# Optimization experiments

Measured on AMD Instinct MI355X. Metric: run time of the kernel, lower is better.

The kernel has to match this reference:

```python
import jax, jax.numpy as jnp
import numpy as np
from jax import lax


def conv2d(x, w, b=None, stride=1, pad=0):
    y = lax.conv_general_dilated(x, w, (stride, stride), [(pad, pad), (pad, pad)],
                                 dimension_numbers=('NCHW', 'OIHW', 'NCHW'))
    if b is not None:
        y = y + b[None, :, None, None]
    return y


def bilinear_resize_ac(S, Ho, Wo):
    # F.interpolate(..., mode='bilinear', align_corners=True)
    B, C, H, W = S.shape
    ys = jnp.linspace(0.0, H - 1.0, Ho)
    xs = jnp.linspace(0.0, W - 1.0, Wo)
    y0 = jnp.floor(ys).astype(jnp.int32); y1 = jnp.minimum(y0 + 1, H - 1); wy = ys - y0
    x0 = jnp.floor(xs).astype(jnp.int32); x1 = jnp.minimum(x0 + 1, W - 1); wx = xs - x0
    Sy = S[:, :, y0, :] * (1 - wy)[None, None, :, None] + S[:, :, y1, :] * wy[None, None, :, None]
    return Sy[:, :, :, x0] * (1 - wx)[None, None, None, :] + Sy[:, :, :, x1] * wx[None, None, None, :]


def deform_conv(x, offset, weight, bias=None, mask=None, stride=1, pad=1, dil=1):
    # (Modulated) deformable conv, deformable_groups=1; DCNv2 semantics:
    # offset channels are (dy, dx) pairs per kernel tap; zero padding outside.
    B, C, H, W = x.shape
    O, Ci, kh, kw = weight.shape
    K = kh * kw
    Ho, Wo = offset.shape[2], offset.shape[3]
    off = offset.reshape(B, K, 2, Ho, Wo)
    kyy, kxx = jnp.meshgrid(jnp.arange(kh) * dil, jnp.arange(kw) * dil, indexing='ij')
    kyy = kyy.reshape(K).astype(x.dtype); kxx = kxx.reshape(K).astype(x.dtype)
    base_y = (jnp.arange(Ho) * stride - pad).astype(x.dtype)
    base_x = (jnp.arange(Wo) * stride - pad).astype(x.dtype)
    py = base_y[None, None, :, None] + kyy[None, :, None, None] + off[:, :, 0]  # [B,K,Ho,Wo]
    px = base_x[None, None, None, :] + kxx[None, :, None, None] + off[:, :, 1]
    y0 = jnp.floor(py); x0 = jnp.floor(px)
    dy = py - y0; dx = px - x0
    y0i = y0.astype(jnp.int32); x0i = x0.astype(jnp.int32)
    xf = x.reshape(B, C, H * W)

    def corner(yi, xi, w):
        valid = (yi >= 0) & (yi <= H - 1) & (xi >= 0) & (xi <= W - 1)
        yc = jnp.clip(yi, 0, H - 1); xc = jnp.clip(xi, 0, W - 1)
        idx = (yc * W + xc).reshape(B, -1)  # [B, K*Ho*Wo]
        g = jax.vmap(lambda f, i: f[:, i])(xf, idx)  # [B, C, K*Ho*Wo]
        g = g.reshape(B, C, K, Ho, Wo)
        return g * (w * valid.astype(x.dtype))[:, None]

    s = (corner(y0i, x0i, (1 - dy) * (1 - dx))
         + corner(y0i, x0i + 1, (1 - dy) * dx)
         + corner(y0i + 1, x0i, dy * (1 - dx))
         + corner(y0i + 1, x0i + 1, dy * dx))  # [B,C,K,Ho,Wo]
    if mask is not None:
        s = s * mask[:, None]  # [B,1,K,Ho,Wo]
    out = jnp.einsum('bckhw,ock->bohw', s, weight.reshape(O, Ci, K))
    if bias is not None:
        out = out + bias[None, :, None, None]
    return out


def setup_inputs():
    key = jax.random.key(0)
    ks = jax.random.split(key, 16)
    B, Cin, Cout, H, W = 8, 256, 256, 64, 64

    def n(k, shape, s):
        return jax.random.normal(k, shape, jnp.float32) * s

    return {
        'x': jax.random.normal(ks[0], (B, Cin, H, W), jnp.float32),
        'S': jax.random.normal(ks[1], (B, 3, 128, 128), jnp.float32),
        'sp_w1': n(ks[2], (64, 3, 3, 3), 0.2), 'sp_b1': jnp.zeros(64), 'sp_s1': jnp.ones(64) + n(ks[3], (64,), 0.05), 'sp_o1': n(ks[3], (64,), 0.05),
        'sp_w2': n(ks[4], (64, 64, 3, 3), 0.05), 'sp_b2': jnp.zeros(64), 'sp_s2': jnp.ones(64) + n(ks[5], (64,), 0.05), 'sp_o2': n(ks[5], (64,), 0.05),
        'sp_w3': n(ks[6], (64, 64, 3, 3), 0.05), 'sp_b3': jnp.zeros(64), 'sp_s3': jnp.ones(64) + n(ks[7], (64,), 0.05), 'sp_o3': n(ks[7], (64,), 0.05),
        'off_w': n(ks[8], (18, 64, 3, 3), 0.05), 'off_b': jnp.zeros(18),
        'dc_off_w': n(ks[9], (18, 64, 3, 3), 0.05), 'dc_off_b': jnp.zeros(18),
        'dc_w': n(ks[10], (64, 64, 3, 3), 0.04),
        'm_w': n(ks[11], (9, 64, 1, 1), 0.1), 'm_b': jnp.zeros(9),
        'weight': n(ks[12], (Cout, Cin, 3, 3), 0.02), 'bias': jnp.zeros(Cout),
    }


def reference(x, S, sp_w1, sp_b1, sp_s1, sp_o1, sp_w2, sp_b2, sp_s2, sp_o2,
              sp_w3, sp_b3, sp_s3, sp_o3, off_w, off_b, dc_off_w, dc_off_b,
              dc_w, m_w, m_b, weight, bias):
    H, W = x.shape[2], x.shape[3]
    Si = bilinear_resize_ac(S, H, W)
    h = jax.nn.relu(conv2d(Si, sp_w1, sp_b1, 1, 1) * sp_s1[None, :, None, None] + sp_o1[None, :, None, None])
    h = jax.nn.relu(conv2d(h, sp_w2, sp_b2, 1, 1) * sp_s2[None, :, None, None] + sp_o2[None, :, None, None])
    h = jax.nn.relu(conv2d(h, sp_w3, sp_b3, 1, 1) * sp_s3[None, :, None, None] + sp_o3[None, :, None, None])
    offset = conv2d(h, off_w, off_b, 1, 1)                 # [B,18,H,W]
    dc_off = conv2d(h, dc_off_w, dc_off_b, 1, 1)           # internal offsets of weight_generator1 (DCNv1)
    feat = deform_conv(h, dc_off, dc_w, None, None, 1, 1, 1)
    mask = jax.nn.sigmoid(conv2d(feat, m_w, m_b, 1, 0))    # [B,9,H,W]
    return deform_conv(x, offset, weight, bias, mask, 1, 1, 1)
```

## Files before the change

kernel.cpp:

```cpp
#include <hip/hip_runtime.h>
#include <hip/hip_bf16.h>

typedef unsigned short u16;
typedef unsigned int u32;
typedef __attribute__((ext_vector_type(8))) short short8;
typedef __attribute__((ext_vector_type(4))) unsigned short ush4;
typedef __attribute__((ext_vector_type(16))) float f32x16;

#define OXT   0
#define OSI   (OXT + 8388608)
#define OA    (OSI + 98304)
#define OB    (OA + 2097152)
#define OC    (OB + 2097152)
#define OOFFS (OC + 2097152)
#define OMSK  (OOFFS + 1179648)
#define OWT   (OMSK + 294912)
#define OWSP1 (OWT + 589824)
#define OBSP1 (OWSP1 + 1728)
#define OWSP2 (OBSP1 + 64)
#define OBSP2 (OWSP2 + 36864)
#define OWSP3 (OBSP2 + 64)
#define OBSP3 (OWSP3 + 36864)
#define OWOFF (OBSP3 + 64)
#define OBOFF (OWOFF + 36864)
#define OWDC  (OBOFF + 64)

__device__ __forceinline__ u16 f2bf(float f) {
    __hip_bfloat16 hb = __float2bfloat16(f);
    return __builtin_bit_cast(u16, hb);
}
__device__ __forceinline__ float bf2f(u16 v) {
    return __builtin_bit_cast(float, (u32)v << 16);
}

__global__ __launch_bounds__(256) void prep_k(
    const float* __restrict__ weight,
    const float* __restrict__ sp_w1, const float* __restrict__ sp_s1,
    const float* __restrict__ sp_w2, const float* __restrict__ sp_s2,
    const float* __restrict__ sp_w3, const float* __restrict__ sp_s3,
    const float* __restrict__ off_w, const float* __restrict__ dc_off_w,
    const float* __restrict__ dc_w,
    const float* __restrict__ sp_b1, const float* __restrict__ sp_o1,
    const float* __restrict__ sp_b2, const float* __restrict__ sp_o2,
    const float* __restrict__ sp_b3, const float* __restrict__ sp_o3,
    const float* __restrict__ off_b, const float* __restrict__ dc_off_b,
    float* __restrict__ ws)
{
    int i = blockIdx.x * 256 + threadIdx.x;
    if (i < 589824) {
        int j = i & 7; int o = (i >> 3) & 255; int kg = i >> 11;
        int K = kg * 8 + j; int k = K >> 8; int c = K & 255;
        ((u16*)(ws + OWT))[i] = f2bf(weight[o * 2304 + c * 9 + k]);
        return;
    }
    i -= 589824;
    if (i < 1728) {
        int o = i & 63; int kc = i >> 6; int c = kc % 3; int k = kc / 3;
        ws[OWSP1 + i] = sp_w1[(o * 3 + c) * 9 + k] * sp_s1[o];
        return;
    }
    i -= 1728;
    if (i < 36864) {
        int e = i & 7; int o = (i >> 3) & 63; int kg = (i >> 9) & 7; int tp = i >> 12;
        ((u16*)(ws + OWSP2))[i] = f2bf(sp_w2[(o * 64 + kg * 8 + e) * 9 + tp] * sp_s2[o]);
        return;
    }
    i -= 36864;
    if (i < 36864) {
        int e = i & 7; int o = (i >> 3) & 63; int kg = (i >> 9) & 7; int tp = i >> 12;
        ((u16*)(ws + OWSP3))[i] = f2bf(sp_w3[(o * 64 + kg * 8 + e) * 9 + tp] * sp_s3[o]);
        return;
    }
    i -= 36864;
    if (i < 36864) {
        int e = i & 7; int o = (i >> 3) & 63; int kg = (i >> 9) & 7; int tp = i >> 12;
        int c = kg * 8 + e;
        float v = 0.f;
        if (o < 18) v = off_w[(o * 64 + c) * 9 + tp];
        else if (o < 36) v = dc_off_w[((o - 18) * 64 + c) * 9 + tp];
        ((u16*)(ws + OWOFF))[i] = f2bf(v);
        return;
    }
    i -= 36864;
    if (i < 36864) {
        int e = i & 7; int o = (i >> 3) & 63; int kg = (i >> 9) & 7; int tp = i >> 12;
        ((u16*)(ws + OWDC))[i] = f2bf(dc_w[(o * 64 + kg * 8 + e) * 9 + tp]);
        return;
    }
    i -= 36864;
    if (i < 64) { ws[OBSP1 + i] = sp_b1[i] * sp_s1[i] + sp_o1[i]; return; }
    i -= 64;
    if (i < 64) { ws[OBSP2 + i] = sp_b2[i] * sp_s2[i] + sp_o2[i]; return; }
    i -= 64;
    if (i < 64) { ws[OBSP3 + i] = sp_b3[i] * sp_s3[i] + sp_o3[i]; return; }
    i -= 64;
    if (i < 64) { ws[OBOFF + i] = (i < 18) ? off_b[i] : (i < 36 ? dc_off_b[i - 18] : 0.f); return; }
}

__global__ __launch_bounds__(256) void transpose_x_k(const float* __restrict__ x,
                                                     u16* __restrict__ xT)
{
    __shared__ float tile[64][65];
    int blk = blockIdx.x;
    int chunk = blk & 3; int by = blk >> 2;
    int b = by >> 6; int y = by & 63;
    int c0 = chunk * 64;
    int t = threadIdx.x;
    for (int i = t; i < 4096; i += 256) {
        int ci = i >> 6, xi = i & 63;
        tile[ci][xi] = x[((b * 256 + c0 + ci) * 64 + y) * 64 + xi];
    }
    __syncthreads();
    for (int i = t; i < 4096; i += 256) {
        int xi = i >> 6, ci = i & 63;
        xT[((b * 64 + y) * 64 + xi) * 256 + c0 + ci] = f2bf(tile[ci][xi]);
    }
}

__global__ __launch_bounds__(256) void resize_k(const float* __restrict__ S,
                                                float* __restrict__ Si)
{
    int i = blockIdx.x * 256 + threadIdx.x;
    if (i >= 8 * 64 * 64 * 3) return;
    int c = i % 3; int x = (i / 3) & 63; int y = (i / 192) & 63; int b = i / 12288;
    const float sc = 127.0f / 63.0f;
    float sy = y * sc, sx = x * sc;
    float fy = floorf(sy), fx = floorf(sx);
    int y0 = (int)fy, x0 = (int)fx;
    int y1 = min(y0 + 1, 127), x1 = min(x0 + 1, 127);
    float wy = sy - fy, wx = sx - fx;
    const float* Sb = S + (size_t)(b * 3 + c) * 16384;
    float v00 = Sb[y0 * 128 + x0], v01 = Sb[y0 * 128 + x1];
    float v10 = Sb[y1 * 128 + x0], v11 = Sb[y1 * 128 + x1];
    Si[i] = (v00 * (1.f - wy) + v10 * wy) * (1.f - wx)
          + (v01 * (1.f - wy) + v11 * wy) * wx;
}

__global__ __launch_bounds__(256) void conv_in_k(const float* __restrict__ in,
                                                 const float* __restrict__ wt,
                                                 const float* __restrict__ bias,
                                                 u16* __restrict__ out)
{
    __shared__ float rows[3][66][3];
    int by = blockIdx.x; int b = by >> 6; int y = by & 63;
    int t = threadIdx.x;
    for (int i = t; i < 3 * 66 * 3; i += 256) {
        int r = i / 198; int rem = i - r * 198;
        int xi = rem / 3; int c = rem - xi * 3;
        int yy = y - 1 + r, xx = xi - 1;
        float v = 0.f;
        if (yy >= 0 && yy < 64 && xx >= 0 && xx < 64)
            v = in[(((b * 64 + yy) * 64 + xx) * 3) + c];
        rows[r][xi][c] = v;
    }
    __syncthreads();
    int o4 = (t & 15) * 4; int xg = t >> 4;
    float acc[4][4];
    #pragma unroll
    for (int oi = 0; oi < 4; oi++) {
        float bv = bias[o4 + oi];
        #pragma unroll
        for (int xi = 0; xi < 4; xi++) acc[oi][xi] = bv;
    }
    for (int k = 0; k < 9; k++) {
        int dy = k / 3, dx = k - 3 * (k / 3);
        for (int c = 0; c < 3; c++) {
            float4 w = *reinterpret_cast<const float4*>(&wt[(k * 3 + c) * 64 + o4]);
            #pragma unroll
            for (int xi = 0; xi < 4; xi++) {
                float iv = rows[dy][xg * 4 + xi + dx][c];
                acc[0][xi] = fmaf(w.x, iv, acc[0][xi]);
                acc[1][xi] = fmaf(w.y, iv, acc[1][xi]);
                acc[2][xi] = fmaf(w.z, iv, acc[2][xi]);
                acc[3][xi] = fmaf(w.w, iv, acc[3][xi]);
            }
        }
    }
    #pragma unroll
    for (int xi = 0; xi < 4; xi++) {
        int x = xg * 4 + xi;
        ush4 v;
        v.x = f2bf(fmaxf(acc[0][xi], 0.f));
        v.y = f2bf(fmaxf(acc[1][xi], 0.f));
        v.z = f2bf(fmaxf(acc[2][xi], 0.f));
        v.w = f2bf(fmaxf(acc[3][xi], 0.f));
        *reinterpret_cast<ush4*>(&out[((size_t)(by * 64 + x)) * 64 + o4]) = v;
    }
}

template <int MODE, bool RELU>
__global__ __launch_bounds__(256) void conv_mfma_k(const u16* __restrict__ in,
                                                   const u16* __restrict__ wm,
                                                   const float* __restrict__ bias,
                                                   u16* __restrict__ outH,
                                                   float* __restrict__ outF)
{
    __shared__ __attribute__((aligned(16))) char lds_h[3 * 66 * 128];
    __shared__ __attribute__((aligned(16))) u16 wtap[2][8][64][8];

    int t = threadIdx.x;
    int b = blockIdx.x >> 6; int y = blockIdx.x & 63;
    int pix0 = b * 4096 + y * 64;
    int wid = t >> 6, lane = t & 63;
    int lrow = lane & 31, lhi = lane >> 5;
    int o0 = (wid & 1) << 5;
    int px0 = (wid >> 1) << 5;
    int px = px0 + lrow;

    for (int i = t; i < 3 * 66 * 8; i += 256) {
        int r = i / 528; int rem = i - r * 528;
        int xi = rem >> 3; int g = rem & 7;
        int yy = y - 1 + r, xx = xi - 1;
        short8 v = {0,0,0,0,0,0,0,0};
        if (yy >= 0 && yy < 64 && xx >= 0 && xx < 64)
            v = *reinterpret_cast<const short8*>(&in[(size_t)((b * 4096 + yy * 64 + xx)) * 64 + g * 8]);
        int byte = (r * 66 + xi) * 128 + ((g * 16) ^ ((xi & 7) << 4));
        *reinterpret_cast<short8*>(lds_h + byte) = v;
    }
    {
        const char* gb = (const char*)(wm);
        char* lb = (char*)&wtap[0][0][0][0];
        #pragma unroll
        for (int i = 0; i < 2; i++) {
            int off = i * 4096 + wid * 1024;
            __builtin_amdgcn_global_load_lds(
                (const __attribute__((address_space(1))) void*)(gb + off + lane * 16),
                (__attribute__((address_space(3))) void*)(lb + off), 16, 0, 0);
        }
    }
    __syncthreads();

    f32x16 acc;
    #pragma unroll
    for (int r = 0; r < 16; r++) acc[r] = 0.f;

    #pragma unroll
    for (int tap = 0; tap < 9; tap++) {
        int cur = tap & 1, nxt = cur ^ 1;
        if (tap < 8) {
            const char* gb = (const char*)(wm + (size_t)(tap + 1) * 4096);
            char* lb = (char*)&wtap[nxt][0][0][0];
            #pragma unroll
            for (int i = 0; i < 2; i++) {
                int off = i * 4096 + wid * 1024;
                __builtin_amdgcn_global_load_lds(
                    (const __attribute__((address_space(1))) void*)(gb + off + lane * 16),
                    (__attribute__((address_space(3))) void*)(lb + off), 16, 0, 0);
            }
        }
        int dy = tap / 3, dx = tap - 3 * (tap / 3);
        int xi = px + dx;
        int rowbyte = (dy * 66 + xi) * 128;
        int swz = (xi & 7) << 4;
        #pragma unroll
        for (int ks = 0; ks < 4; ks++) {
            int kg = ks * 2 + lhi;
            short8 a0 = *reinterpret_cast<const short8*>(&wtap[cur][kg][o0 + lrow][0]);
            short8 b0 = *reinterpret_cast<const short8*>(lds_h + rowbyte + ((kg * 16) ^ swz));
            acc = __builtin_amdgcn_mfma_f32_32x32x16_bf16(a0, b0, acc, 0, 0, 0);
        }
        if (tap < 8) asm volatile("s_waitcnt vmcnt(0)" ::: "memory");
        __builtin_amdgcn_s_barrier();
    }
    __syncthreads();

    if (MODE == 0) {
        #pragma unroll
        for (int q = 0; q < 4; q++) {
            int ob = o0 + q * 8 + 4 * lhi;
            #pragma unroll
            for (int h = 0; h < 2; h++) {
                float v0 = acc[q * 4 + h * 2] + bias[ob + h * 2];
                float v1 = acc[q * 4 + h * 2 + 1] + bias[ob + h * 2 + 1];
                if (RELU) { v0 = fmaxf(v0, 0.f); v1 = fmaxf(v1, 0.f); }
                u32 pk = (u32)f2bf(v0) | ((u32)f2bf(v1) << 16);
                int byte = px * 128 + (((ob + h * 2) * 2) ^ ((px & 7) << 4));
                *reinterpret_cast<u32*>(lds_h + byte) = pk;
            }
        }
        __syncthreads();
        #pragma unroll
        for (int i = 0; i < 2; i++) {
            int cid = i * 256 + t;
            int p = cid >> 3, g = cid & 7;
            short8 v = *reinterpret_cast<const short8*>(lds_h + p * 128 + ((g * 16) ^ ((p & 7) << 4)));
            *reinterpret_cast<short8*>(&outH[(size_t)(pix0 + p) * 64 + g * 8]) = v;
        }
    } else {
        float* ltf = (float*)lds_h;
        #pragma unroll
        for (int r = 0; r < 16; r++) {
            int o = o0 + (r & 3) + ((r >> 2) << 3) + (lhi << 2);
            if (o < 36) ltf[px * 40 + o] = acc[r] + bias[o];
        }
        __syncthreads();
        for (int i = t; i < 576; i += 256) {
            int p = i / 9, q = i - 9 * (i / 9);
            float4 v = *reinterpret_cast<const float4*>(&ltf[p * 40 + q * 4]);
            *reinterpret_cast<float4*>(&outF[(size_t)(pix0 + p) * 36 + q * 4]) = v;
        }
    }
}

__global__ __launch_bounds__(512) void dconv_small_mfma(
    const u16* __restrict__ h, const float* __restrict__ offs,
    const u16* __restrict__ wdc, const float* __restrict__ m_w,
    const float* __restrict__ m_b, float* __restrict__ maskb)
{
    __shared__ __attribute__((aligned(16))) char smem[33280];
    u16 (*wtile)[8][64][8] = (u16 (*)[8][64][8])smem;
    u16 (*stile)[128][8]   = (u16 (*)[128][8])(smem + 16384);

    int t = threadIdx.x;
    int id = blockIdx.x;
    int blk = (id & 7) * 32 + (id >> 3);
    int pix0 = blk * 128;
    int b = pix0 >> 12;
    int wid = t >> 6, lane = t & 63;
    int lrow = lane & 31, lhi = lane >> 5;
    int o0 = (wid & 1) << 5;
    int px0 = (wid >> 1) << 5;
    int gp = t >> 2, gsub = t & 3;

    {
        const char* gb = (const char*)wdc;
        char* lb = (char*)&wtile[0][0][0][0];
        __builtin_amdgcn_global_load_lds(
            (const __attribute__((address_space(1))) void*)(gb + wid * 1024 + lane * 16),
            (__attribute__((address_space(3))) void*)(lb + wid * 1024), 16, 0, 0);
    }
    __syncthreads();

    f32x16 acc;
    #pragma unroll
    for (int r = 0; r < 16; r++) acc[r] = 0.f;

    int car[4]; float cwr[4];

    for (int tap = 0; tap < 9; ++tap) {
        int cur = tap & 1, nxt = cur ^ 1;
        {
            int pix = pix0 + gp; int pib = pix & 4095;
            int y = pib >> 6, x = pib & 63;
            float offy = offs[(size_t)pix * 36 + 18 + tap * 2];
            float offx = offs[(size_t)pix * 36 + 18 + tap * 2 + 1];
            float py = (float)(y - 1 + tap / 3) + offy;
            float pxf = (float)(x - 1 + (tap % 3)) + offx;
            float fy = floorf(py), fx = floorf(pxf);
            int y0 = (int)fy, x0 = (int)fx;
            float dyf = py - fy, dxf = pxf - fx;
            #pragma unroll
            for (int j = 0; j < 4; j++) {
                float wj = ((j >> 1) ? dyf : 1.f - dyf) * ((j & 1) ? dxf : 1.f - dxf);
                int yy = y0 + (j >> 1), xx = x0 + (j & 1);
                bool valid = (yy >= 0 && yy < 64 && xx >= 0 && xx < 64);
                int yc = min(max(yy, 0), 63), xc = min(max(xx, 0), 63);
                car[j] = (b * 4096 + yc * 64 + xc) << 6;
                cwr[j] = valid ? wj : 0.f;
            }
        }
        int c = gsub << 4;
        float va[16];
        #pragma unroll
        for (int e = 0; e < 16; e++) va[e] = 0.f;
        #pragma unroll
        for (int j = 0; j < 4; j++) {
            float w = cwr[j];
            const u16* p = h + car[j] + c;
            short8 r0 = *reinterpret_cast<const short8*>(p);
            short8 r1 = *reinterpret_cast<const short8*>(p + 8);
            #pragma unroll
            for (int e = 0; e < 8; e++) {
                va[e]     = fmaf(w, bf2f((u16)r0[e]), va[e]);
                va[8 + e] = fmaf(w, bf2f((u16)r1[e]), va[8 + e]);
            }
        }
        if (tap < 8) {
            const char* gb = (const char*)(wdc + (size_t)(tap + 1) * 4096);
            char* lb = (char*)&wtile[nxt][0][0][0];
            __builtin_amdgcn_global_load_lds(
                (const __attribute__((address_space(1))) void*)(gb + wid * 1024 + lane * 16),
                (__attribute__((address_space(3))) void*)(lb + wid * 1024), 16, 0, 0);
        }
        short8 s0, s1;
        #pragma unroll
        for (int e = 0; e < 8; e++) { s0[e] = (short)f2bf(va[e]); s1[e] = (short)f2bf(va[8 + e]); }
        *reinterpret_cast<short8*>(&stile[gsub * 2][gp][0]) = s0;
        *reinterpret_cast<short8*>(&stile[gsub * 2 + 1][gp][0]) = s1;

        if (tap < 8) asm volatile("s_waitcnt vmcnt(1) lgkmcnt(0)" ::: "memory");
        else         asm volatile("s_waitcnt vmcnt(0) lgkmcnt(0)" ::: "memory");
        __builtin_amdgcn_s_barrier();

        #pragma unroll
        for (int ks = 0; ks < 4; ks++) {
            int kg = ks * 2 + lhi;
            short8 a0 = *reinterpret_cast<const short8*>(&wtile[cur][kg][o0 + lrow][0]);
            short8 b0 = *reinterpret_cast<const short8*>(&stile[kg][px0 + lrow][0]);
            acc = __builtin_amdgcn_mfma_f32_32x32x16_bf16(a0, b0, acc, 0, 0, 0);
        }
        asm volatile("s_waitcnt lgkmcnt(0)" ::: "memory");
        __builtin_amdgcn_s_barrier();
    }

    __syncthreads();
    float* featl = (float*)smem;
    int pxl = px0 + lrow;
    #pragma unroll
    for (int r = 0; r < 16; r++) {
        int o = o0 + (r & 3) + ((r >> 2) << 3) + (lhi << 2);
        featl[pxl * 65 + o] = acc[r];
    }
    __syncthreads();
    if (t < 256) {
        int p = t >> 1, hh = t & 1;
        int pix = pix0 + p;
        const float* fr = &featl[p * 65];
        int j0 = hh ? 4 : 0, j1 = hh ? 9 : 4;
        for (int j = j0; j < j1; j++) {
            float a = m_b[j];
            #pragma unroll 8
            for (int cc = 0; cc < 64; cc++) a = fmaf(fr[cc], m_w[j * 64 + cc], a);
            maskb[(size_t)pix * 9 + j] = 1.f / (1.f + expf(-a));
        }
    }
}

__global__ __launch_bounds__(512) void dconv_big_mfma(
    const u16* __restrict__ xT, const float* __restrict__ offs,
    const float* __restrict__ maskb, const u16* __restrict__ wKg,
    const float* __restrict__ bias, float* __restrict__ out)
{
    __shared__ __attribute__((aligned(16))) u16 wtile[2][8][256][8];
    __shared__ __attribute__((aligned(16))) u16 stile[8][64][8];

    int t = threadIdx.x;
    int id = blockIdx.x;
    int blk = (id & 7) * 64 + (id >> 3);
    int pix0 = blk * 64;
    int b = pix0 >> 12, pib0 = pix0 & 4095;
    int wid = t >> 6, lane = t & 63;
    int lrow = lane & 31, lhi = lane >> 5;
    int o0 = wid << 5;
    int gp = t >> 3, gsub = t & 7;

    {
        const char* gb = (const char*)wKg;
        char* lb = (char*)&wtile[0][0][0][0];
        #pragma unroll
        for (int i = 0; i < 4; i++) {
            int off = i * 8192 + wid * 1024;
            __builtin_amdgcn_global_load_lds(
                (const __attribute__((address_space(1))) void*)(gb + off + lane * 16),
                (__attribute__((address_space(3))) void*)(lb + off), 16, 0, 0);
        }
    }
    __syncthreads();

    f32x16 acc[2];
    #pragma unroll
    for (int fp = 0; fp < 2; fp++)
        #pragma unroll
        for (int r = 0; r < 16; r++) acc[fp][r] = 0.f;

    int car[4]; float cwr[4];

    for (int kt = 0; kt < 36; ++kt) {
        int cur = kt & 1, nxt = cur ^ 1;
        int tap = kt >> 2, chunk = kt & 3;

        if (chunk == 0) {
            int pix = pix0 + gp; int pib = pix & 4095;
            int y = pib >> 6, x = pib & 63;
            float offy = offs[(size_t)pix * 36 + tap * 2];
            float offx = offs[(size_t)pix * 36 + tap * 2 + 1];
            float m = maskb[(size_t)pix * 9 + tap];
            float py = (float)(y - 1 + tap / 3) + offy;
            float pxf = (float)(x - 1 + (tap % 3)) + offx;
            float fy = floorf(py), fx = floorf(pxf);
            int y0 = (int)fy, x0 = (int)fx;
            float dyf = py - fy, dxf = pxf - fx;
            #pragma unroll
            for (int j = 0; j < 4; j++) {
                float wj = ((j >> 1) ? dyf : 1.f - dyf) * ((j & 1) ? dxf : 1.f - dxf);
                int yy = y0 + (j >> 1), xx = x0 + (j & 1);
                bool valid = (yy >= 0 && yy < 64 && xx >= 0 && xx < 64);
                int yc = min(max(yy, 0), 63), xc = min(max(xx, 0), 63);
                car[j] = (b * 4096 + yc * 64 + xc) << 8;
                cwr[j] = valid ? wj * m : 0.f;
            }
        }

        int c = (chunk << 6) + (gsub << 3);
        float va[8];
        #pragma unroll
        for (int e = 0; e < 8; e++) va[e] = 0.f;
        #pragma unroll
        for (int j = 0; j < 4; j++) {
            float w = cwr[j];
            short8 r0 = *reinterpret_cast<const short8*>(xT + car[j] + c);
            #pragma unroll
            for (int e = 0; e < 8; e++) va[e] = fmaf(w, bf2f((u16)r0[e]), va[e]);
        }
        if (kt < 35) {
            const char* gb = (const char*)(wKg + (size_t)(kt + 1) * 16384);
            char* lb = (char*)&wtile[nxt][0][0][0];
            #pragma unroll
            for (int i = 0; i < 4; i++) {
                int off = i * 8192 + wid * 1024;
                __builtin_amdgcn_global_load_lds(
                    (const __attribute__((address_space(1))) void*)(gb + off + lane * 16),
                    (__attribute__((address_space(3))) void*)(lb + off), 16, 0, 0);
            }
        }
        short8 s0;
        #pragma unroll
        for (int e = 0; e < 8; e++) s0[e] = (short)f2bf(va[e]);
        *reinterpret_cast<short8*>(&stile[gsub][gp][0]) = s0;

        if (kt < 35) asm volatile("s_waitcnt vmcnt(4) lgkmcnt(0)" ::: "memory");
        else         asm volatile("s_waitcnt vmcnt(0) lgkmcnt(0)" ::: "memory");
        __builtin_amdgcn_s_barrier();

        #pragma unroll
        for (int ks = 0; ks < 4; ks++) {
            int kg = ks * 2 + lhi;
            short8 a0 = *reinterpret_cast<const short8*>(&wtile[cur][kg][o0 + lrow][0]);
            short8 b0 = *reinterpret_cast<const short8*>(&stile[kg][lrow][0]);
            short8 b1 = *reinterpret_cast<const short8*>(&stile[kg][32 + lrow][0]);
            acc[0] = __builtin_amdgcn_mfma_f32_32x32x16_bf16(a0, b0, acc[0], 0, 0, 0);
            acc[1] = __builtin_amdgcn_mfma_f32_32x32x16_bf16(a0, b1, acc[1], 0, 0, 0);
        }
        asm volatile("s_waitcnt lgkmcnt(0)" ::: "memory");
        __builtin_amdgcn_s_barrier();
    }

    #pragma unroll
    for (int fp = 0; fp < 2; fp++) {
        #pragma unroll
        for (int r = 0; r < 16; r++) {
            int o = o0 + (r & 3) + ((r >> 2) << 3) + (lhi << 2);
            size_t rowoff = ((size_t)(b * 256 + o) << 12) + pib0;
            out[rowoff + fp * 32 + lrow] = acc[fp][r] + bias[o];
        }
    }
}

extern "C" void kernel_launch(void* const* d_in, const int* in_sizes, int n_in,
                              void* d_out, int out_size, void* d_ws, size_t ws_size,
                              hipStream_t stream)
{
    const float* x        = (const float*)d_in[0];
    const float* S        = (const float*)d_in[1];
    const float* sp_w1    = (const float*)d_in[2];
    const float* sp_b1    = (const float*)d_in[3];
    const float* sp_s1    = (const float*)d_in[4];
    const float* sp_o1    = (const float*)d_in[5];
    const float* sp_w2    = (const float*)d_in[6];
    const float* sp_b2    = (const float*)d_in[7];
    const float* sp_s2    = (const float*)d_in[8];
    const float* sp_o2    = (const float*)d_in[9];
    const float* sp_w3    = (const float*)d_in[10];
    const float* sp_b3    = (const float*)d_in[11];
    const float* sp_s3    = (const float*)d_in[12];
    const float* sp_o3    = (const float*)d_in[13];
    const float* off_w    = (const float*)d_in[14];
    const float* off_b    = (const float*)d_in[15];
    const float* dc_off_w = (const float*)d_in[16];
    const float* dc_off_b = (const float*)d_in[17];
    const float* dc_w     = (const float*)d_in[18];
    const float* m_w      = (const float*)d_in[19];
    const float* m_b      = (const float*)d_in[20];
    const float* weight   = (const float*)d_in[21];
    const float* bias     = (const float*)d_in[22];
    float* out = (float*)d_out;
    float* ws  = (float*)d_ws;

    u16*   xTb   = (u16*)(ws + OXT);
    float* Si    = ws + OSI;
    u16*   h1    = (u16*)(ws + OA);
    u16*   h2    = (u16*)(ws + OB);
    u16*   h3    = (u16*)(ws + OC);
    float* offsb = ws + OOFFS;
    float* maskb = ws + OMSK;

    prep_k<<<2888, 256, 0, stream>>>(weight, sp_w1, sp_s1, sp_w2, sp_s2, sp_w3, sp_s3,
                                     off_w, dc_off_w, dc_w,
                                     sp_b1, sp_o1, sp_b2, sp_o2, sp_b3, sp_o3,
                                     off_b, dc_off_b, ws);
    transpose_x_k<<<2048, 256, 0, stream>>>(x, xTb);
    resize_k<<<384, 256, 0, stream>>>(S, Si);
    conv_in_k<<<512, 256, 0, stream>>>(Si, ws + OWSP1, ws + OBSP1, h1);
    conv_mfma_k<0, true><<<512, 256, 0, stream>>>(h1, (const u16*)(ws + OWSP2),
                                                  ws + OBSP2, h2, nullptr);
    conv_mfma_k<0, true><<<512, 256, 0, stream>>>(h2, (const u16*)(ws + OWSP3),
                                                  ws + OBSP3, h3, nullptr);
    conv_mfma_k<1, false><<<512, 256, 0, stream>>>(h3, (const u16*)(ws + OWOFF),
                                                   ws + OBOFF, nullptr, offsb);
    dconv_small_mfma<<<256, 512, 0, stream>>>(h3, offsb, (const u16*)(ws + OWDC),
                                              m_w, m_b, maskb);
    dconv_big_mfma<<<512, 512, 0, stream>>>(xTb, offsb, maskb,
                                            (const u16*)(ws + OWT), bias, out);
}
```

Baseline: 149.6 us.

## Double-buffer sample tiles, drop a barrier per step, and XOR-swizzle LDS rows

In both deformable-conv MFMA kernels the sampled-input LDS tile is now double-buffered. This allows one barrier per K step instead of two, and the initial __syncthreads is removed. The weight prefetch for the next step is issued after the MFMAs rather than before the sample-tile store. Sample-tile rows are XOR-swizzled by k-group to reduce LDS bank conflicts on the MFMA B-operand reads. The cost is more LDS per block and a full vmcnt(0) wait each step, which may reduce overlap of the weight prefetch with the gather.

Result: no change. 147.5 us, median of 4 (-1.4%).

```diff
diff --git a/kernel.cpp b/kernel.cpp
--- a/kernel.cpp
+++ b/kernel.cpp
@@ -32,6 +32,9 @@
 __device__ __forceinline__ float bf2f(u16 v) {
     return __builtin_bit_cast(float, (u32)v << 16);
 }
+__device__ __forceinline__ int sswz(int kg, int px) {
+    return (px & ~7) | ((px ^ kg) & 7);
+}
 
 __global__ __launch_bounds__(256) void prep_k(
     const float* __restrict__ weight,
@@ -307,9 +310,9 @@
     const u16* __restrict__ wdc, const float* __restrict__ m_w,
     const float* __restrict__ m_b, float* __restrict__ maskb)
 {
-    __shared__ __attribute__((aligned(16))) char smem[33280];
-    u16 (*wtile)[8][64][8] = (u16 (*)[8][64][8])smem;
-    u16 (*stile)[128][8]   = (u16 (*)[128][8])(smem + 16384);
+    __shared__ __attribute__((aligned(16))) char smem[49152];
+    u16 (*wtile)[8][64][8]  = (u16 (*)[8][64][8])smem;
+    u16 (*stile)[8][128][8] = (u16 (*)[8][128][8])(smem + 16384);
 
     int t = threadIdx.x;
     int id = blockIdx.x;
@@ -329,7 +332,6 @@
             (const __attribute__((address_space(1))) void*)(gb + wid * 1024 + lane * 16),
             (__attribute__((address_space(3))) void*)(lb + wid * 1024), 16, 0, 0);
     }
-    __syncthreads();
 
     f32x16 acc;
     #pragma unroll
@@ -375,6 +377,23 @@
                 va[8 + e] = fmaf(w, bf2f((u16)r1[e]), va[8 + e]);
             }
         }
+        short8 s0, s1;
+        #pragma unroll
+        for (int e = 0; e < 8; e++) { s0[e] = (short)f2bf(va[e]); s1[e] = (short)f2bf(va[8 + e]); }
+        int kg0 = gsub * 2, kg1 = gsub * 2 + 1;
+        *reinterpret_cast<short8*>(&stile[cur][kg0][sswz(kg0, gp)][0]) = s0;
+        *reinterpret_cast<short8*>(&stile[cur][kg1][sswz(kg1, gp)][0]) = s1;
+
+        asm volatile("s_waitcnt vmcnt(0) lgkmcnt(0)" ::: "memory");
+        __builtin_amdgcn_s_barrier();
+
+        #pragma unroll
+        for (int ks = 0; ks < 4; ks++) {
+            int kg = ks * 2 + lhi;
+            short8 a0 = *reinterpret_cast<const short8*>(&wtile[cur][kg][o0 + lrow][0]);
+            short8 b0 = *reinterpret_cast<const short8*>(&stile[cur][kg][sswz(kg, px0 + lrow)][0]);
+            acc = __builtin_amdgcn_mfma_f32_32x32x16_bf16(a0, b0, acc, 0, 0, 0);
+        }
         if (tap < 8) {
             const char* gb = (const char*)(wdc + (size_t)(tap + 1) * 4096);
             char* lb = (char*)&wtile[nxt][0][0][0];
@@ -382,25 +401,6 @@
                 (const __attribute__((address_space(1))) void*)(gb + wid * 1024 + lane * 16),
                 (__attribute__((address_space(3))) void*)(lb + wid * 1024), 16, 0, 0);
         }
-        short8 s0, s1;
-        #pragma unroll
-        for (int e = 0; e < 8; e++) { s0[e] = (short)f2bf(va[e]); s1[e] = (short)f2bf(va[8 + e]); }
-        *reinterpret_cast<short8*>(&stile[gsub * 2][gp][0]) = s0;
-        *reinterpret_cast<short8*>(&stile[gsub * 2 + 1][gp][0]) = s1;
-
-        if (tap < 8) asm volatile("s_waitcnt vmcnt(1) lgkmcnt(0)" ::: "memory");
-        else         asm volatile("s_waitcnt vmcnt(0) lgkmcnt(0)" ::: "memory");
-        __builtin_amdgcn_s_barrier();
-
-        #pragma unroll
-        for (int ks = 0; ks < 4; ks++) {
-            int kg = ks * 2 + lhi;
-            short8 a0 = *reinterpret_cast<const short8*>(&wtile[cur][kg][o0 + lrow][0]);
-            short8 b0 = *reinterpret_cast<const short8*>(&stile[kg][px0 + lrow][0]);
-            acc = __builtin_amdgcn_mfma_f32_32x32x16_bf16(a0, b0, acc, 0, 0, 0);
-        }
-        asm volatile("s_waitcnt lgkmcnt(0)" ::: "memory");
-        __builtin_amdgcn_s_barrier();
     }
 
     __syncthreads();
@@ -432,7 +432,7 @@
     const float* __restrict__ bias, float* __restrict__ out)
 {
     __shared__ __attribute__((aligned(16))) u16 wtile[2][8][256][8];
-    __shared__ __attribute__((aligned(16))) u16 stile[8][64][8];
+    __shared__ __attribute__((aligned(16))) u16 stile[2][8][64][8];
 
     int t = threadIdx.x;
     int id = blockIdx.x;
@@ -455,7 +455,6 @@
                 (__attribute__((address_space(3))) void*)(lb + off), 16, 0, 0);
         }
     }
-    __syncthreads();
 
     f32x16 acc[2];
     #pragma unroll
@@ -502,6 +501,23 @@
             #pragma unroll
             for (int e = 0; e < 8; e++) va[e] = fmaf(w, bf2f((u16)r0[e]), va[e]);
         }
+        short8 s0;
+        #pragma unroll
+        for (int e = 0; e < 8; e++) s0[e] = (short)f2bf(va[e]);
+        *reinterpret_cast<short8*>(&stile[cur][gsub][sswz(gsub, gp)][0]) = s0;
+
+        asm volatile("s_waitcnt vmcnt(0) lgkmcnt(0)" ::: "memory");
+        __builtin_amdgcn_s_barrier();
+
+        #pragma unroll
+        for (int ks = 0; ks < 4; ks++) {
+            int kg = ks * 2 + lhi;
+            short8 a0 = *reinterpret_cast<const short8*>(&wtile[cur][kg][o0 + lrow][0]);
+            short8 b0 = *reinterpret_cast<const short8*>(&stile[cur][kg][sswz(kg, lrow)][0]);
+            short8 b1 = *reinterpret_cast<const short8*>(&stile[cur][kg][sswz(kg, 32 + lrow)][0]);
+            acc[0] = __builtin_amdgcn_mfma_f32_32x32x16_bf16(a0, b0, acc[0], 0, 0, 0);
+            acc[1] = __builtin_amdgcn_mfma_f32_32x32x16_bf16(a0, b1, acc[1], 0, 0, 0);
+        }
         if (kt < 35) {
             const char* gb = (const char*)(wKg + (size_t)(kt + 1) * 16384);
             char* lb = (char*)&wtile[nxt][0][0][0];
@@ -513,26 +529,6 @@
                     (__attribute__((address_space(3))) void*)(lb + off), 16, 0, 0);
             }
         }
-        short8 s0;
-        #pragma unroll
-        for (int e = 0; e < 8; e++) s0[e] = (short)f2bf(va[e]);
-        *reinterpret_cast<short8*>(&stile[gsub][gp][0]) = s0;
-
-        if (kt < 35) asm volatile("s_waitcnt vmcnt(4) lgkmcnt(0)" ::: "memory");
-        else         asm volatile("s_waitcnt vmcnt(0) lgkmcnt(0)" ::: "memory");
-        __builtin_amdgcn_s_barrier();
-
-        #pragma unroll
-        for (int ks = 0; ks < 4; ks++) {
-            int kg = ks * 2 + lhi;
-            short8 a0 = *reinterpret_cast<const short8*>(&wtile[cur][kg][o0 + lrow][0]);
-            short8 b0 = *reinterpret_cast<const short8*>(&stile[kg][lrow][0]);
-            short8 b1 = *reinterpret_cast<const short8*>(&stile[kg][32 + lrow][0]);
-            acc[0] = __builtin_amdgcn_mfma_f32_32x32x16_bf16(a0, b0, acc[0], 0, 0, 0);
-            acc[1] = __builtin_amdgcn_mfma_f32_32x32x16_bf16(a0, b1, acc[1], 0, 0, 0);
-        }
-        asm volatile("s_waitcnt lgkmcnt(0)" ::: "memory");
-        __builtin_amdgcn_s_barrier();
     }
 
     #pragma unroll
```
